# Optimization experiments

Measured on AMD Instinct MI355X. Metric: run time of the kernel, lower is better.

Reference implementation:

```python
import jax, jax.numpy as jnp
import numpy as np

NUM_USERS = 100000
NUM_ITEMS = 100000
N = NUM_USERS + NUM_ITEMS
D = 64
E = 1200000


def setup_inputs() -> dict:
    key = jax.random.key(0)
    k1, k2, k3, k4, k5 = jax.random.split(key, 5)
    edge_index = jax.random.randint(k1, (2, E), 0, N, dtype=jnp.int64)
    user_emb = jax.random.normal(k2, (NUM_USERS, D), dtype=jnp.float32)
    item_emb = jax.random.normal(k3, (NUM_ITEMS, D), dtype=jnp.float32)
    W1 = jax.random.normal(k4, (D, D), dtype=jnp.float32) / np.sqrt(D)
    b1 = jnp.zeros((D,), dtype=jnp.float32)
    W2 = jax.random.normal(k5, (D, D), dtype=jnp.float32) / np.sqrt(D)
    b2 = jnp.zeros((D,), dtype=jnp.float32)
    return {"edge_index": edge_index, "user_emb": user_emb, "item_emb": item_emb,
            "W1": W1, "b1": b1, "W2": W2, "b2": b2}


def _gcn_conv(x, row, col, norm, W, b, n_nodes):
    # x: [N, D]; row/col: [E+N] (with self-loops); norm: [E+N]
    x = x @ W                                  # linear transform (no bias in lin)
    msg = x[row] * norm[:, None]               # gather + scale (memory-bound)
    out = jax.ops.segment_sum(msg, col, num_segments=n_nodes)  # scatter-add
    return out + b


def reference(edge_index, user_emb, item_emb, W1, b1, W2, b2):
    x = jnp.concatenate([user_emb, item_emb], axis=0)  # [N, D]
    n_nodes = x.shape[0]
    # gcn_norm: add self-loops, symmetric deg^{-1/2} normalization
    sl = jnp.arange(n_nodes, dtype=edge_index.dtype)
    row = jnp.concatenate([edge_index[0], sl])
    col = jnp.concatenate([edge_index[1], sl])
    deg = jax.ops.segment_sum(jnp.ones_like(col, dtype=x.dtype), col,
                              num_segments=n_nodes)
    dinv = jnp.where(deg > 0, jax.lax.rsqrt(jnp.maximum(deg, 1e-12)), 0.0)
    norm = dinv[row] * dinv[col]
    x = _gcn_conv(x, row, col, norm, W1, b1, n_nodes)
    x = _gcn_conv(x, row, col, norm, W2, b2, n_nodes)
    return x
```

## Files before the change

### kernel.cpp

```cpp
#include <hip/hip_runtime.h>

#define DIM 64
#define GPW 4
#define BSHIFT 9
#define BSPAN 512
#define MAXNB 512

typedef __attribute__((ext_vector_type(8))) __bf16 bf16x8;
typedef __attribute__((ext_vector_type(4))) __bf16 bf16x4;
typedef __attribute__((ext_vector_type(4))) float f32x4;

__device__ __forceinline__ f32x4 mfma16(bf16x8 a, bf16x8 b, f32x4 c) {
    return __builtin_amdgcn_mfma_f32_16x16x32_bf16(a, b, c, 0, 0, 0);
}

__device__ __forceinline__ float bf2f(unsigned short u) {
    return __uint_as_float((unsigned)u << 16);
}


__global__ void zerob_kernel(int* __restrict__ b) { b[threadIdx.x] = 0; }

__global__ __launch_bounds__(512) void bucket_count_kernel(
    const int* __restrict__ ei, int* __restrict__ bcnt, int E_, int NB) {
    __shared__ int hist[MAXNB];
    int tid = threadIdx.x;
    for (int i = tid; i < NB; i += 512) hist[i] = 0;
    __syncthreads();
    int chunk = (E_ + gridDim.x - 1) / gridDim.x;
    int e0 = blockIdx.x * chunk, e1 = min(E_, e0 + chunk);
    for (int e = e0 + tid; e < e1; e += 512)
        atomicAdd(&hist[ei[E_ + e] >> BSHIFT], 1);
    __syncthreads();
    for (int i = tid; i < NB; i += 512)
        if (hist[i]) atomicAdd(&bcnt[i], hist[i]);
}

__global__ __launch_bounds__(512) void bucket_scan_kernel(
    const int* __restrict__ bcnt, int* __restrict__ bptr, int* __restrict__ bcur,
    int* __restrict__ rowptr, int NB, int N_, int E_) {
    __shared__ int sm[512];
    int tid = threadIdx.x;
    int v = (tid < NB) ? bcnt[tid] : 0;
    sm[tid] = v;
    __syncthreads();
    for (int off = 1; off < 512; off <<= 1) {
        int t = 0;
        if (tid >= off) t = sm[tid - off];
        __syncthreads();
        if (tid >= off) sm[tid] += t;
        __syncthreads();
    }
    if (tid < NB) {
        int ex = sm[tid] - v;
        bptr[tid] = ex;
        bcur[tid] = ex;
    }
    if (tid == 0) { bptr[NB] = E_; rowptr[N_] = E_; }
}

__global__ __launch_bounds__(512) void scatter_kernel(
    const int* __restrict__ ei, int* __restrict__ bcur,
    unsigned* __restrict__ packed, int E_, int NB) {
    __shared__ int h[MAXNB];
    int tid = threadIdx.x;
    int chunk = (E_ + gridDim.x - 1) / gridDim.x;
    int e0 = blockIdx.x * chunk, e1 = min(E_, e0 + chunk);
    for (int i = tid; i < NB; i += 512) h[i] = 0;
    __syncthreads();
    for (int e = e0 + tid; e < e1; e += 512)
        atomicAdd(&h[ei[E_ + e] >> BSHIFT], 1);
    __syncthreads();
    for (int i = tid; i < NB; i += 512) {
        int c = h[i];
        h[i] = c ? atomicAdd(&bcur[i], c) : 0;
    }
    __syncthreads();
    for (int e = e0 + tid; e < e1; e += 512) {
        int s = ei[e], d = ei[E_ + e];
        int b = d >> BSHIFT;
        int pos = atomicAdd(&h[b], 1);
        packed[pos] = ((unsigned)s << BSHIFT) | (unsigned)(d & (BSPAN - 1));
    }
}

__global__ __launch_bounds__(256) void bucket_sort_kernel(
    const unsigned* __restrict__ packed, const int* __restrict__ bptr,
    int* __restrict__ rowptr, int* __restrict__ srcs,
    float* __restrict__ dinv, int N_) {
    __shared__ int cnt[BSPAN];
    __shared__ int sc[256];
    int tid = threadIdx.x;
    int b = blockIdx.x;
    int beg = bptr[b], end = bptr[b + 1];
    int node0 = b << BSHIFT;
    int nn = min(BSPAN, N_ - node0);
    cnt[tid] = 0; cnt[tid + 256] = 0;
    __syncthreads();
    for (int i = beg + tid; i < end; i += 256)
        atomicAdd(&cnt[packed[i] & (BSPAN - 1)], 1);
    __syncthreads();
    int degA = cnt[tid], degB = cnt[tid + 256];
    int a0 = cnt[2 * tid], a1 = cnt[2 * tid + 1];
    if (tid < nn) dinv[node0 + tid] = rsqrtf((float)(1 + degA));
    if (tid + 256 < nn) dinv[node0 + tid + 256] = rsqrtf((float)(1 + degB));
    int tot = a0 + a1;
    sc[tid] = tot;
    __syncthreads();
    for (int off = 1; off < 256; off <<= 1) {
        int t = 0;
        if (tid >= off) t = sc[tid - off];
        __syncthreads();
        if (tid >= off) sc[tid] += t;
        __syncthreads();
    }
    int ex = sc[tid] - tot;
    cnt[2 * tid] = ex;
    cnt[2 * tid + 1] = ex + a0;
    __syncthreads();
    if (tid < nn) rowptr[node0 + tid] = beg + cnt[tid];
    if (tid + 256 < nn) rowptr[node0 + tid + 256] = beg + cnt[tid + 256];
    __syncthreads();
    for (int i = beg + tid; i < end; i += 256) {
        unsigned p = packed[i];
        int pos = atomicAdd(&cnt[p & (BSPAN - 1)], 1);
        srcs[beg + pos] = (int)(p >> BSHIFT);
    }
}


template <bool BF16IN>
__global__ __launch_bounds__(256) void gemm_kernel(
    const void* __restrict__ xa_, const void* __restrict__ xb_, int split,
    const float* __restrict__ W, const float* __restrict__ dinv,
    __bf16* __restrict__ h, int n, int ngroups) {
    int lane = threadIdx.x & 63;
    int q = lane >> 4, t = lane & 15;
    int wv = __builtin_amdgcn_readfirstlane(threadIdx.x >> 6);
    int g0 = (blockIdx.x * 4 + wv) * GPW;
    if (g0 >= ngroups) return;

    bf16x8 Bf[4][2];
#pragma unroll
    for (int nt = 0; nt < 4; ++nt)
#pragma unroll
        for (int kt = 0; kt < 2; ++kt) {
            bf16x8 f;
#pragma unroll
            for (int j = 0; j < 8; ++j)
                f[j] = (__bf16)W[(kt * 32 + q * 8 + j) * DIM + nt * 16 + t];
            Bf[nt][kt] = f;
        }

    auto loadA = [&](int r0, f32x4* raw) {
        int row = r0 + t;
        if (row >= n) row = n - 1;
        if constexpr (BF16IN) {
            const __bf16* xr = (const __bf16*)xa_ + (size_t)row * DIM;
            raw[0] = *(const f32x4*)(xr + q * 8);
            raw[1] = *(const f32x4*)(xr + 32 + q * 8);
        } else {
            const float* xr = (row < split)
                ? ((const float*)xa_ + (size_t)row * DIM)
                : ((const float*)xb_ + (size_t)(row - split) * DIM);
            raw[0] = *(const f32x4*)(xr + q * 8);
            raw[1] = *(const f32x4*)(xr + q * 8 + 4);
            raw[2] = *(const f32x4*)(xr + 32 + q * 8);
            raw[3] = *(const f32x4*)(xr + 32 + q * 8 + 4);
        }
    };

    f32x4 cur[4];
    loadA(g0 * 16, cur);

#pragma unroll 1
    for (int gi = 0; gi < GPW; ++gi) {
        int g = g0 + gi;
        if (g >= ngroups) break;
        int r0 = g * 16;
        f32x4 nxt[4];
        bool pf = (gi + 1 < GPW) && (g + 1 < ngroups);
        if (pf) loadA(r0 + 16, nxt);

        bf16x8 A0, A1;
        if constexpr (BF16IN) {
            A0 = __builtin_bit_cast(bf16x8, cur[0]);
            A1 = __builtin_bit_cast(bf16x8, cur[1]);
        } else {
#pragma unroll
            for (int j = 0; j < 4; ++j) {
                A0[j] = (__bf16)cur[0][j]; A0[j + 4] = (__bf16)cur[1][j];
                A1[j] = (__bf16)cur[2][j]; A1[j + 4] = (__bf16)cur[3][j];
            }
        }

        f32x4 z = {0.f, 0.f, 0.f, 0.f};
        f32x4 acc[4];
#pragma unroll
        for (int nt = 0; nt < 4; ++nt)
            acc[nt] = mfma16(A1, Bf[nt][1], mfma16(A0, Bf[nt][0], z));

        f32x4 d4 = *(const f32x4*)(dinv + r0 + q * 4);
#pragma unroll
        for (int nt = 0; nt < 4; ++nt)
#pragma unroll
            for (int reg = 0; reg < 4; ++reg) {
                int row = r0 + q * 4 + reg;
                if (row < n)
                    h[(size_t)row * DIM + nt * 16 + t] =
                        (__bf16)(acc[nt][reg] * d4[reg]);
            }
#pragma unroll
        for (int i = 0; i < 4; ++i) cur[i] = nxt[i];
    }
}

template <typename OutT>
__global__ __launch_bounds__(256) void agg_kernel(
    const int* __restrict__ rowptr, const int* __restrict__ srcs,
    const __bf16* __restrict__ h, const float* __restrict__ bias,
    const float* __restrict__ dinv, OutT* __restrict__ out, int n) {
    int lane = threadIdx.x & 63;
    int grp = lane >> 4;
    int t4 = lane & 15;
    int node = blockIdx.x * 4 + __builtin_amdgcn_readfirstlane(threadIdx.x >> 6);
    if (node >= n) return;
    int beg = rowptr[node], end = rowptr[node + 1];

    float a0 = 0.f, a1 = 0.f, a2 = 0.f, a3 = 0.f;
    for (int base = beg - 1; base < end; base += 8) {
        int i0 = base + grp;
        int i1 = i0 + 4;
        int s0 = node;
        if (i0 >= beg && i0 < end) s0 = srcs[i0];
        int s1 = 0;
        if (i1 < end) s1 = srcs[i1];
        ushort4 v0 = make_ushort4(0, 0, 0, 0);
        ushort4 v1 = make_ushort4(0, 0, 0, 0);
        if (i0 < end)
            v0 = *(const ushort4*)(h + (size_t)s0 * DIM + t4 * 4);
        if (i1 < end)
            v1 = *(const ushort4*)(h + (size_t)s1 * DIM + t4 * 4);
        a0 += bf2f(v0.x) + bf2f(v1.x);
        a1 += bf2f(v0.y) + bf2f(v1.y);
        a2 += bf2f(v0.z) + bf2f(v1.z);
        a3 += bf2f(v0.w) + bf2f(v1.w);
    }
#pragma unroll
    for (int off = 16; off <= 32; off <<= 1) {
        a0 += __shfl_xor(a0, off);
        a1 += __shfl_xor(a1, off);
        a2 += __shfl_xor(a2, off);
        a3 += __shfl_xor(a3, off);
    }
    float dn = dinv[node];
    f32x4 bv = *(const f32x4*)(bias + t4 * 4);
    float r0 = fmaf(dn, a0, bv[0]);
    float r1 = fmaf(dn, a1, bv[1]);
    float r2 = fmaf(dn, a2, bv[2]);
    float r3 = fmaf(dn, a3, bv[3]);
    if (grp == 0) {
        if constexpr (sizeof(OutT) == 4) {
            f32x4 r = {r0, r1, r2, r3};
            *(f32x4*)((float*)out + (size_t)node * DIM + t4 * 4) = r;
        } else {
            bf16x4 r;
            r[0] = (__bf16)r0; r[1] = (__bf16)r1;
            r[2] = (__bf16)r2; r[3] = (__bf16)r3;
            *(bf16x4*)((__bf16*)out + (size_t)node * DIM + t4 * 4) = r;
        }
    }
}

static inline size_t align16(size_t x) { return (x + 15) & ~(size_t)15; }

extern "C" void kernel_launch(void* const* d_in, const int* in_sizes, int n_in,
                              void* d_out, int out_size, void* d_ws, size_t ws_size,
                              hipStream_t stream) {
    const int* ei         = (const int*)d_in[0];
    const float* user_emb = (const float*)d_in[1];
    const float* item_emb = (const float*)d_in[2];
    const float* W1 = (const float*)d_in[3];
    const float* b1 = (const float*)d_in[4];
    const float* W2 = (const float*)d_in[5];
    const float* b2 = (const float*)d_in[6];
    float* out = (float*)d_out;

    const int E_ = in_sizes[0] / 2;
    const int NU = in_sizes[1] / DIM;
    const int NI = in_sizes[2] / DIM;
    const int N_ = NU + NI;
    const int NB = (N_ + BSPAN - 1) >> BSHIFT;

    char* p = (char*)d_ws;
    int* srcs   = (int*)p;                   p += align16((size_t)E_ * 4);
    __bf16* h   = (__bf16*)p;                p += align16((size_t)N_ * DIM * 2);
    __bf16* t1  = (__bf16*)p;                p += align16((size_t)N_ * DIM * 2);
    float* dinv = (float*)p;                 p += align16((size_t)N_ * 4);
    int* rowptr = (int*)p;                   p += align16((size_t)(N_ + 1) * 4);
    int* bcnt   = (int*)p;                   p += align16((size_t)MAXNB * 4);
    int* bptr   = (int*)p;                   p += align16((size_t)(MAXNB + 1) * 4);
    int* bcur   = (int*)p;                   p += align16((size_t)MAXNB * 4);
    unsigned* packed = (unsigned*)t1;

    zerob_kernel<<<1, MAXNB, 0, stream>>>(bcnt);
    bucket_count_kernel<<<256, 512, 0, stream>>>(ei, bcnt, E_, NB);
    bucket_scan_kernel<<<1, 512, 0, stream>>>(bcnt, bptr, bcur, rowptr, NB, N_, E_);
    scatter_kernel<<<256, 512, 0, stream>>>(ei, bcur, packed, E_, NB);
    bucket_sort_kernel<<<NB, 256, 0, stream>>>(packed, bptr, rowptr, srcs, dinv, N_);

    int NG = (N_ + 15) / 16;
    int gblocks = (NG + 4 * GPW - 1) / (4 * GPW);
    int ablocks = (N_ + 3) / 4;

    gemm_kernel<false><<<gblocks, 256, 0, stream>>>(user_emb, item_emb, NU,
                                                    W1, dinv, h, N_, NG);
    agg_kernel<__bf16><<<ablocks, 256, 0, stream>>>(rowptr, srcs, h, b1, dinv, t1, N_);
    gemm_kernel<true><<<gblocks, 256, 0, stream>>>(t1, t1, N_,
                                                   W2, dinv, h, N_, NG);
    agg_kernel<float><<<ablocks, 256, 0, stream>>>(rowptr, srcs, h, b2, dinv, out, N_);
}
```

Measured before the change: 302.5 us.

## Fold both GCN linear layers into one precomputed weight and single final GEMM

The two-layer GCN has no nonlinearity, so the output is rewritten as A·A·X·(W1·W2) + (A·1)·(b1·W2) + b2. A small prep kernel precomputes W1·W2 and b1·W2. The pipeline becomes a cast-and-scale pass, two sparse aggregations (the first also accumulates the row sums of normalized adjacency weights), and one MFMA GEMM that applies the bias terms. This removes one GEMM pass and its intermediate round trip through memory. The aggregation loop also issues four gathers per iteration instead of two to expose more memory-level parallelism. In exchange it adds a single-block serial weight-product kernel and reorders bf16 rounding, which can change numerical error.

```diff
diff --git a/kernel.cpp b/kernel.cpp
--- a/kernel.cpp
+++ b/kernel.cpp
@@ -129,122 +129,77 @@
 }
 
 
-template <bool BF16IN>
-__global__ __launch_bounds__(256) void gemm_kernel(
-    const void* __restrict__ xa_, const void* __restrict__ xb_, int split,
-    const float* __restrict__ W, const float* __restrict__ dinv,
-    __bf16* __restrict__ h, int n, int ngroups) {
-    int lane = threadIdx.x & 63;
-    int q = lane >> 4, t = lane & 15;
-    int wv = __builtin_amdgcn_readfirstlane(threadIdx.x >> 6);
-    int g0 = (blockIdx.x * 4 + wv) * GPW;
-    if (g0 >= ngroups) return;
-
-    bf16x8 Bf[4][2];
-#pragma unroll
-    for (int nt = 0; nt < 4; ++nt)
-#pragma unroll
-        for (int kt = 0; kt < 2; ++kt) {
-            bf16x8 f;
-#pragma unroll
-            for (int j = 0; j < 8; ++j)
-                f[j] = (__bf16)W[(kt * 32 + q * 8 + j) * DIM + nt * 16 + t];
-            Bf[nt][kt] = f;
-        }
-
-    auto loadA = [&](int r0, f32x4* raw) {
-        int row = r0 + t;
-        if (row >= n) row = n - 1;
-        if constexpr (BF16IN) {
-            const __bf16* xr = (const __bf16*)xa_ + (size_t)row * DIM;
-            raw[0] = *(const f32x4*)(xr + q * 8);
-            raw[1] = *(const f32x4*)(xr + 32 + q * 8);
-        } else {
-            const float* xr = (row < split)
-                ? ((const float*)xa_ + (size_t)row * DIM)
-                : ((const float*)xb_ + (size_t)(row - split) * DIM);
-            raw[0] = *(const f32x4*)(xr + q * 8);
-            raw[1] = *(const f32x4*)(xr + q * 8 + 4);
-            raw[2] = *(const f32x4*)(xr + 32 + q * 8);
-            raw[3] = *(const f32x4*)(xr + 32 + q * 8 + 4);
-        }
-    };
-
-    f32x4 cur[4];
-    loadA(g0 * 16, cur);
-
-#pragma unroll 1
-    for (int gi = 0; gi < GPW; ++gi) {
-        int g = g0 + gi;
-        if (g >= ngroups) break;
-        int r0 = g * 16;
-        f32x4 nxt[4];
-        bool pf = (gi + 1 < GPW) && (g + 1 < ngroups);
-        if (pf) loadA(r0 + 16, nxt);
-
-        bf16x8 A0, A1;
-        if constexpr (BF16IN) {
-            A0 = __builtin_bit_cast(bf16x8, cur[0]);
-            A1 = __builtin_bit_cast(bf16x8, cur[1]);
-        } else {
-#pragma unroll
-            for (int j = 0; j < 4; ++j) {
-                A0[j] = (__bf16)cur[0][j]; A0[j + 4] = (__bf16)cur[1][j];
-                A1[j] = (__bf16)cur[2][j]; A1[j + 4] = (__bf16)cur[3][j];
-            }
-        }
-
-        f32x4 z = {0.f, 0.f, 0.f, 0.f};
-        f32x4 acc[4];
-#pragma unroll
-        for (int nt = 0; nt < 4; ++nt)
-            acc[nt] = mfma16(A1, Bf[nt][1], mfma16(A0, Bf[nt][0], z));
-
-        f32x4 d4 = *(const f32x4*)(dinv + r0 + q * 4);
-#pragma unroll
-        for (int nt = 0; nt < 4; ++nt)
-#pragma unroll
-            for (int reg = 0; reg < 4; ++reg) {
-                int row = r0 + q * 4 + reg;
-                if (row < n)
-                    h[(size_t)row * DIM + nt * 16 + t] =
-                        (__bf16)(acc[nt][reg] * d4[reg]);
-            }
-#pragma unroll
-        for (int i = 0; i < 4; ++i) cur[i] = nxt[i];
-    }
-}
-
-template <typename OutT>
+__global__ __launch_bounds__(256) void prep_kernel(
+    const float* __restrict__ W1, const float* __restrict__ W2,
+    const float* __restrict__ b1, float* __restrict__ Wp,
+    float* __restrict__ c) {
+    int t = threadIdx.x;
+#pragma unroll
+    for (int e = 0; e < 16; ++e) {
+        int idx = t * 16 + e;
+        int k = idx >> 6, n = idx & 63;
+        float s = 0.f;
+        for (int m = 0; m < 64; ++m) s = fmaf(W1[k * 64 + m], W2[m * 64 + n], s);
+        Wp[idx] = s;
+    }
+    if (t < 64) {
+        float s = 0.f;
+        for (int k = 0; k < 64; ++k) s = fmaf(b1[k], W2[k * 64 + t], s);
+        c[t] = s;
+    }
+}
+
+__global__ __launch_bounds__(256) void cast_kernel(
+    const float* __restrict__ ua, const float* __restrict__ ub, int split,
+    const float* __restrict__ dinv, __bf16* __restrict__ g, int n) {
+    int idx = blockIdx.x * 256 + threadIdx.x;
+    int row = idx >> 3, off = (idx & 7) * 8;
+    if (row >= n) return;
+    const float* x = (row < split) ? ua + (size_t)row * DIM
+                                   : ub + (size_t)(row - split) * DIM;
+    float dn = dinv[row];
+    f32x4 v0 = *(const f32x4*)(x + off);
+    f32x4 v1 = *(const f32x4*)(x + off + 4);
+    bf16x8 o;
+#pragma unroll
+    for (int j = 0; j < 4; ++j) {
+        o[j]     = (__bf16)(v0[j] * dn);
+        o[j + 4] = (__bf16)(v1[j] * dn);
+    }
+    *(bf16x8*)(g + (size_t)row * DIM + off) = o;
+}
+
+template <bool FIRST>
 __global__ __launch_bounds__(256) void agg_kernel(
     const int* __restrict__ rowptr, const int* __restrict__ srcs,
-    const __bf16* __restrict__ h, const float* __restrict__ bias,
-    const float* __restrict__ dinv, OutT* __restrict__ out, int n) {
+    const __bf16* __restrict__ in, const float* __restrict__ dinv,
+    __bf16* __restrict__ outrow, float* __restrict__ r, int n) {
     int lane = threadIdx.x & 63;
     int grp = lane >> 4;
     int t4 = lane & 15;
     int node = blockIdx.x * 4 + __builtin_amdgcn_readfirstlane(threadIdx.x >> 6);
     if (node >= n) return;
     int beg = rowptr[node], end = rowptr[node + 1];
-
-    float a0 = 0.f, a1 = 0.f, a2 = 0.f, a3 = 0.f;
-    for (int base = beg - 1; base < end; base += 8) {
-        int i0 = base + grp;
-        int i1 = i0 + 4;
-        int s0 = node;
-        if (i0 >= beg && i0 < end) s0 = srcs[i0];
-        int s1 = 0;
-        if (i1 < end) s1 = srcs[i1];
-        ushort4 v0 = make_ushort4(0, 0, 0, 0);
-        ushort4 v1 = make_ushort4(0, 0, 0, 0);
-        if (i0 < end)
-            v0 = *(const ushort4*)(h + (size_t)s0 * DIM + t4 * 4);
-        if (i1 < end)
-            v1 = *(const ushort4*)(h + (size_t)s1 * DIM + t4 * 4);
-        a0 += bf2f(v0.x) + bf2f(v1.x);
-        a1 += bf2f(v0.y) + bf2f(v1.y);
-        a2 += bf2f(v0.z) + bf2f(v1.z);
-        a3 += bf2f(v0.w) + bf2f(v1.w);
+    float dn = dinv[node];
+
+    float a0 = 0.f, a1 = 0.f, a2 = 0.f, a3 = 0.f, sd = 0.f;
+    for (int base = beg - 1; base < end; base += 16) {
+#pragma unroll
+        for (int k = 0; k < 4; ++k) {
+            int i = base + grp + 4 * k;
+            int s = node;
+            if (i >= beg && i < end) s = srcs[i];
+            ushort4 v = make_ushort4(0, 0, 0, 0);
+            float dv = 0.f;
+            if (i < end) {
+                v = *(const ushort4*)(in + (size_t)s * DIM + t4 * 4);
+                if constexpr (FIRST)
+                    if (t4 == 0) dv = dinv[s];
+            }
+            a0 += bf2f(v.x); a1 += bf2f(v.y);
+            a2 += bf2f(v.z); a3 += bf2f(v.w);
+            if constexpr (FIRST) sd += dv;
+        }
     }
 #pragma unroll
     for (int off = 16; off <= 32; off <<= 1) {
@@ -252,23 +207,87 @@
         a1 += __shfl_xor(a1, off);
         a2 += __shfl_xor(a2, off);
         a3 += __shfl_xor(a3, off);
-    }
-    float dn = dinv[node];
-    f32x4 bv = *(const f32x4*)(bias + t4 * 4);
-    float r0 = fmaf(dn, a0, bv[0]);
-    float r1 = fmaf(dn, a1, bv[1]);
-    float r2 = fmaf(dn, a2, bv[2]);
-    float r3 = fmaf(dn, a3, bv[3]);
+        if constexpr (FIRST) sd += __shfl_xor(sd, off);
+    }
+    float scale = FIRST ? dn * dn : dn;
     if (grp == 0) {
-        if constexpr (sizeof(OutT) == 4) {
-            f32x4 r = {r0, r1, r2, r3};
-            *(f32x4*)((float*)out + (size_t)node * DIM + t4 * 4) = r;
-        } else {
-            bf16x4 r;
-            r[0] = (__bf16)r0; r[1] = (__bf16)r1;
-            r[2] = (__bf16)r2; r[3] = (__bf16)r3;
-            *(bf16x4*)((__bf16*)out + (size_t)node * DIM + t4 * 4) = r;
+        bf16x4 o;
+        o[0] = (__bf16)(a0 * scale); o[1] = (__bf16)(a1 * scale);
+        o[2] = (__bf16)(a2 * scale); o[3] = (__bf16)(a3 * scale);
+        *(bf16x4*)(outrow + (size_t)node * DIM + t4 * 4) = o;
+        if constexpr (FIRST)
+            if (t4 == 0) r[node] = dn * sd;
+    }
+}
+
+__global__ __launch_bounds__(256) void gemm_kernel(
+    const __bf16* __restrict__ z, const float* __restrict__ Wp,
+    const float* __restrict__ c, const float* __restrict__ b2,
+    const float* __restrict__ r, float* __restrict__ out, int n, int ngroups) {
+    int lane = threadIdx.x & 63;
+    int q = lane >> 4, t = lane & 15;
+    int wv = __builtin_amdgcn_readfirstlane(threadIdx.x >> 6);
+    int g0 = (blockIdx.x * 4 + wv) * GPW;
+    if (g0 >= ngroups) return;
+
+    bf16x8 Bf[4][2];
+#pragma unroll
+    for (int nt = 0; nt < 4; ++nt)
+#pragma unroll
+        for (int kt = 0; kt < 2; ++kt) {
+            bf16x8 f;
+#pragma unroll
+            for (int j = 0; j < 8; ++j)
+                f[j] = (__bf16)Wp[(kt * 32 + q * 8 + j) * DIM + nt * 16 + t];
+            Bf[nt][kt] = f;
         }
+    float cv[4], bv[4];
+#pragma unroll
+    for (int nt = 0; nt < 4; ++nt) {
+        cv[nt] = c[nt * 16 + t];
+        bv[nt] = b2[nt * 16 + t];
+    }
+
+    auto loadA = [&](int r0, f32x4* raw) {
+        int row = r0 + t;
+        if (row >= n) row = n - 1;
+        const __bf16* xr = z + (size_t)row * DIM;
+        raw[0] = *(const f32x4*)(xr + q * 8);
+        raw[1] = *(const f32x4*)(xr + 32 + q * 8);
+    };
+
+    f32x4 cur[2];
+    loadA(g0 * 16, cur);
+
+#pragma unroll 1
+    for (int gi = 0; gi < GPW; ++gi) {
+        int g = g0 + gi;
+        if (g >= ngroups) break;
+        int r0 = g * 16;
+        f32x4 nxt[2];
+        bool pf = (gi + 1 < GPW) && (g + 1 < ngroups);
+        if (pf) loadA(r0 + 16, nxt);
+
+        bf16x8 A0 = __builtin_bit_cast(bf16x8, cur[0]);
+        bf16x8 A1 = __builtin_bit_cast(bf16x8, cur[1]);
+
+        f32x4 zf = {0.f, 0.f, 0.f, 0.f};
+        f32x4 acc[4];
+#pragma unroll
+        for (int nt = 0; nt < 4; ++nt)
+            acc[nt] = mfma16(A1, Bf[nt][1], mfma16(A0, Bf[nt][0], zf));
+
+        f32x4 r4 = *(const f32x4*)(r + r0 + q * 4);
+#pragma unroll
+        for (int nt = 0; nt < 4; ++nt)
+#pragma unroll
+            for (int reg = 0; reg < 4; ++reg) {
+                int row = r0 + q * 4 + reg;
+                if (row < n)
+                    out[(size_t)row * DIM + nt * 16 + t] =
+                        acc[nt][reg] + fmaf(r4[reg], cv[nt], bv[nt]);
+            }
+        cur[0] = nxt[0]; cur[1] = nxt[1];
     }
 }
 
@@ -291,32 +310,37 @@
     const int NI = in_sizes[2] / DIM;
     const int N_ = NU + NI;
     const int NB = (N_ + BSPAN - 1) >> BSHIFT;
+    const int NG = (N_ + 15) / 16;
+    const int NP = NG * 16;
 
     char* p = (char*)d_ws;
-    int* srcs   = (int*)p;                   p += align16((size_t)E_ * 4);
-    __bf16* h   = (__bf16*)p;                p += align16((size_t)N_ * DIM * 2);
-    __bf16* t1  = (__bf16*)p;                p += align16((size_t)N_ * DIM * 2);
-    float* dinv = (float*)p;                 p += align16((size_t)N_ * 4);
-    int* rowptr = (int*)p;                   p += align16((size_t)(N_ + 1) * 4);
-    int* bcnt   = (int*)p;                   p += align16((size_t)MAXNB * 4);
-    int* bptr   = (int*)p;                   p += align16((size_t)(MAXNB + 1) * 4);
-    int* bcur   = (int*)p;                   p += align16((size_t)MAXNB * 4);
-    unsigned* packed = (unsigned*)t1;
+    int* srcs   = (int*)p;               p += align16((size_t)E_ * 4);
+    __bf16* g   = (__bf16*)p;            p += align16((size_t)NP * DIM * 2);
+    __bf16* q   = (__bf16*)p;            p += align16((size_t)NP * DIM * 2);
+    float* dinv = (float*)p;             p += align16((size_t)NP * 4);
+    float* rvec = (float*)p;             p += align16((size_t)NP * 4);
+    int* rowptr = (int*)p;               p += align16((size_t)(N_ + 1) * 4);
+    int* bcnt   = (int*)p;               p += align16((size_t)MAXNB * 4);
+    int* bptr   = (int*)p;               p += align16((size_t)(MAXNB + 1) * 4);
+    int* bcur   = (int*)p;               p += align16((size_t)MAXNB * 4);
+    float* Wp   = (float*)p;             p += align16((size_t)DIM * DIM * 4);
+    float* cvec = (float*)p;             p += align16((size_t)DIM * 4);
+    __bf16* zrow = g;
+    unsigned* packed = (unsigned*)q;
 
     zerob_kernel<<<1, MAXNB, 0, stream>>>(bcnt);
     bucket_count_kernel<<<256, 512, 0, stream>>>(ei, bcnt, E_, NB);
     bucket_scan_kernel<<<1, 512, 0, stream>>>(bcnt, bptr, bcur, rowptr, NB, N_, E_);
     scatter_kernel<<<256, 512, 0, stream>>>(ei, bcur, packed, E_, NB);
     bucket_sort_kernel<<<NB, 256, 0, stream>>>(packed, bptr, rowptr, srcs, dinv, N_);
-
-    int NG = (N_ + 15) / 16;
+    prep_kernel<<<1, 256, 0, stream>>>(W1, W2, b1, Wp, cvec);
+
+    int cblocks = ((N_ * 8) + 255) / 256;
+    int ablocks = (N_ + 3) / 4;
     int gblocks = (NG + 4 * GPW - 1) / (4 * GPW);
-    int ablocks = (N_ + 3) / 4;
-
-    gemm_kernel<false><<<gblocks, 256, 0, stream>>>(user_emb, item_emb, NU,
-                                                    W1, dinv, h, N_, NG);
-    agg_kernel<__bf16><<<ablocks, 256, 0, stream>>>(rowptr, srcs, h, b1, dinv, t1, N_);
-    gemm_kernel<true><<<gblocks, 256, 0, stream>>>(t1, t1, N_,
-                                                   W2, dinv, h, N_, NG);
-    agg_kernel<float><<<ablocks, 256, 0, stream>>>(rowptr, srcs, h, b2, dinv, out, N_);
-}
+
+    cast_kernel<<<cblocks, 256, 0, stream>>>(user_emb, item_emb, NU, dinv, g, N_);
+    agg_kernel<true><<<ablocks, 256, 0, stream>>>(rowptr, srcs, g, dinv, q, rvec, N_);
+    agg_kernel<false><<<ablocks, 256, 0, stream>>>(rowptr, srcs, q, dinv, zrow, nullptr, N_);
+    gemm_kernel<<<gblocks, 256, 0, stream>>>(zrow, Wp, cvec, b2, rvec, out, N_, NG);
+}
```

New measurement: 347.5 us. 14.9% more time.
